# Optimization experiments

Hardware: AMD Instinct MI355X
Metric: run time of the kernel (lower is better)

Reference implementation:

```python
import math
import jax, jax.numpy as jnp
import numpy as np

H = 64  # lstm_hidden_size
T = 9   # seq_len


def _lstm_layer(pre, w_hh):
    """pre: [N, T, 4H] = x @ W_ih^T + b_ih + b_hh; w_hh: [4H, H].
    Returns full hidden sequence [N, T, H]. Gate order (PyTorch): i, f, g, o."""
    N = pre.shape[0]
    pre_t = jnp.transpose(pre, (1, 0, 2))  # [T, N, 4H]
    h0 = jnp.zeros((N, H), dtype=pre.dtype)
    c0 = jnp.zeros((N, H), dtype=pre.dtype)

    def step(carry, xt):
        h, c = carry
        g = xt + h @ w_hh.T  # [N, 4H]
        i = jax.nn.sigmoid(g[:, 0 * H:1 * H])
        f = jax.nn.sigmoid(g[:, 1 * H:2 * H])
        gg = jnp.tanh(g[:, 2 * H:3 * H])
        o = jax.nn.sigmoid(g[:, 3 * H:4 * H])
        c = f * c + i * gg
        h = o * jnp.tanh(c)
        return (h, c), h

    _, hs = jax.lax.scan(step, (h0, c0), pre_t)  # hs: [T, N, H]
    return jnp.transpose(hs, (1, 0, 2))  # [N, T, H]


def _forward(xy, w_ih0, w_hh0, b0, w_ih1, w_hh1, b1,
             fus_w, fus_b, res_w1, res_b1, res_w2, res_b2,
             head_w1, head_b1, head_w2, head_b2):
    x = xy[:, 0:1]
    y = xy[:, 1:2]
    pi = math.pi
    # seq: [N, 9, 1]
    seq = jnp.stack([x, y, x ** 2, y ** 2, x * y,
                     jnp.sin(pi * x), jnp.cos(pi * x),
                     jnp.sin(pi * y), jnp.cos(pi * y)], axis=1)
    # layer 0: input size 1
    pre0 = jnp.einsum('ntd,gd->ntg', seq, w_ih0) + b0  # [N, T, 4H]
    h_seq0 = _lstm_layer(pre0, w_hh0)                   # [N, T, H]
    # layer 1: input size H
    pre1 = jnp.einsum('nth,gh->ntg', h_seq0, w_ih1) + b1
    h_seq1 = _lstm_layer(pre1, w_hh1)
    feat = h_seq1[:, -1, :]                             # [N, H]

    fused = jnp.concatenate([feat, xy], axis=1)         # [N, H+2]
    z = jnp.tanh(fused @ fus_w.T + fus_b)               # [N, 64]
    for k in range(res_w1.shape[0]):
        t = jnp.tanh(z @ res_w1[k].T + res_b1[k])
        z = z + jnp.tanh(t @ res_w2[k].T + res_b2[k])
    h = jnp.tanh(z @ head_w1.T + head_b1)
    return h @ head_w2.T + head_b2                      # [N, 5]


def setup_inputs() -> dict:
    key = jax.random.key(0)
    ks = jax.random.split(key, 20)
    N = 262144
    D = 64  # fc_hidden_dim
    xy = jax.random.uniform(ks[0], (N, 2), dtype=jnp.float32)

    def w(k, shape, scale=0.1):
        return (jax.random.normal(k, shape, dtype=jnp.float32) * scale)

    inp = {
        'xy': xy,
        'w_ih0': w(ks[1], (4 * H, 1)),
        'w_hh0': w(ks[2], (4 * H, H)),
        'b0': jnp.zeros((4 * H,), jnp.float32),
        'w_ih1': w(ks[3], (4 * H, H)),
        'w_hh1': w(ks[4], (4 * H, H)),
        'b1': jnp.zeros((4 * H,), jnp.float32),
        'fus_w': w(ks[5], (D, H + 2)),
        'fus_b': jnp.zeros((D,), jnp.float32),
        'res_w1': w(ks[6], (3, D, D)),
        'res_b1': jnp.zeros((3, D), jnp.float32),
        'res_w2': w(ks[7], (3, D, D)),
        'res_b2': jnp.zeros((3, D), jnp.float32),
        'head_w1': w(ks[8], (D, D)),
        'head_b1': jnp.zeros((D,), jnp.float32),
        'head_w2': w(ks[9], (5, D)),
        'head_b2': jnp.zeros((5,), jnp.float32),
    }
    return inp


def reference(xy, w_ih0, w_hh0, b0, w_ih1, w_hh1, b1,
              fus_w, fus_b, res_w1, res_b1, res_w2, res_b2,
              head_w1, head_b1, head_w2, head_b2):
    return _forward(xy, w_ih0, w_hh0, b0, w_ih1, w_hh1, b1,
                    fus_w, fus_b, res_w1, res_b1, res_w2, res_b2,
                    head_w1, head_b1, head_w2, head_b2)
```

## Files before the change

### kernel.cpp

```cpp
#include <hip/hip_runtime.h>
#include <math.h>

#define PI_F 3.14159265358979323846f
#define WAVES 12
#define TPB (WAVES*64)
#define TPB2 512

typedef _Float16 half_t;
typedef __attribute__((ext_vector_type(8))) _Float16 f16x8;
typedef __attribute__((ext_vector_type(4))) float f32x4;

union F16x8U { f16x8 v; unsigned int u[4]; half_t h[8]; };

__device__ __forceinline__ float frcp(float x)  { return __builtin_amdgcn_rcpf(x); }
__device__ __forceinline__ float fsig(float x)  { return frcp(1.0f + __expf(-x)); }
__device__ __forceinline__ float ftanh(float x) { return 1.0f - 2.0f * frcp(1.0f + __expf(2.0f * x)); }

#define MFMA16(a,b,c) __builtin_amdgcn_mfma_f32_16x16x32_f16((a),(b),(c),0,0,0)

#define AUG_B   98304
#define B1_B    99328
#define EPI_H   50176
#define BIAS_B  172032
#define HOUT_H  88064
#define EF_FUS  0
#define EF_R1   6144
#define EF_R2   18432
#define EF_HW1  30720
#define EF_HW2  34816

__global__ void pack_weights(const float* __restrict__ w_ih0, const float* __restrict__ w_hh0, const float* __restrict__ b0,
                             const float* __restrict__ w_ih1, const float* __restrict__ w_hh1, const float* __restrict__ b1,
                             const float* __restrict__ fus_w, const float* __restrict__ fus_b,
                             const float* __restrict__ res_w1, const float* __restrict__ res_b1,
                             const float* __restrict__ res_w2, const float* __restrict__ res_b2,
                             const float* __restrict__ head_w1, const float* __restrict__ head_b1,
                             const float* __restrict__ head_w2, const float* __restrict__ head_b2,
                             half_t* __restrict__ hws)
{
    int id = blockIdx.x * blockDim.x + threadIdx.x;

    if (id < 6144) {
        int ln = id & 63, rest = id >> 6;
        int kb = rest & 1, cb = (rest >> 1) & 15, mat = rest >> 5;
        const float* W = (mat == 0) ? w_hh0 : ((mat == 1) ? w_ih1 : w_hh1);
        const float* src = W + (cb * 16 + (ln & 15)) * 64 + kb * 32 + (ln >> 4) * 8;
        F16x8U t;
        #pragma unroll
        for (int i = 0; i < 8; ++i) t.h[i] = (half_t)src[i];
        *(f16x8*)&hws[id * 8] = t.v;
        return;
    }
    id -= 6144;
    if (id < 256) {
        F16x8U t; t.u[0] = 0;
        t.h[0] = (half_t)w_ih0[id];
        t.h[1] = (half_t)b0[id];
        ((unsigned int*)((char*)hws + AUG_B))[id] = t.u[0];
        return;
    }
    id -= 256;
    if (id < 256) {
        ((float*)((char*)hws + B1_B))[id] = b1[id];
        return;
    }
    id -= 256;
    if (id < 768) {
        int ln = id & 63, rest = id >> 6;
        int kb = rest % 3, cb = rest / 3;
        int col = cb * 16 + (ln & 15), q = ln >> 4;
        F16x8U t; t.u[0] = t.u[1] = t.u[2] = t.u[3] = 0;
        if (kb < 2) {
            #pragma unroll
            for (int i = 0; i < 8; ++i) t.h[i] = (half_t)fus_w[col * 66 + kb * 32 + q * 8 + i];
        } else if (q == 0) {
            t.h[0] = (half_t)fus_w[col * 66 + 64];
            t.h[1] = (half_t)fus_w[col * 66 + 65];
            t.h[2] = (half_t)fus_b[col];
        }
        *(f16x8*)&hws[(EPI_H + EF_FUS + id * 8)] = t.v;
        return;
    }
    id -= 768;
    if (id < 1536) {
        int ln = id & 63, rest = id >> 6;
        int kb = rest & 1, cb = (rest >> 1) & 3, rb = rest >> 3;
        int col = cb * 16 + (ln & 15), q = ln >> 4;
        F16x8U t;
        #pragma unroll
        for (int i = 0; i < 8; ++i) t.h[i] = (half_t)res_w1[rb * 4096 + col * 64 + kb * 32 + q * 8 + i];
        *(f16x8*)&hws[(EPI_H + EF_R1 + id * 8)] = t.v;
        return;
    }
    id -= 1536;
    if (id < 1536) {
        int ln = id & 63, rest = id >> 6;
        int kb = rest & 1, cb = (rest >> 1) & 3, rb = rest >> 3;
        int col = cb * 16 + (ln & 15), q = ln >> 4;
        F16x8U t;
        #pragma unroll
        for (int i = 0; i < 8; ++i) t.h[i] = (half_t)res_w2[rb * 4096 + col * 64 + kb * 32 + q * 8 + i];
        *(f16x8*)&hws[(EPI_H + EF_R2 + id * 8)] = t.v;
        return;
    }
    id -= 1536;
    if (id < 512) {
        int ln = id & 63, rest = id >> 6;
        int kb = rest & 1, cb = rest >> 1;
        int col = cb * 16 + (ln & 15), q = ln >> 4;
        F16x8U t;
        #pragma unroll
        for (int i = 0; i < 8; ++i) t.h[i] = (half_t)head_w1[col * 64 + kb * 32 + q * 8 + i];
        *(f16x8*)&hws[(EPI_H + EF_HW1 + id * 8)] = t.v;
        return;
    }
    id -= 512;
    if (id < 128) {
        int ln = id & 63, kb = id >> 6;
        int col = ln & 15, q = ln >> 4;
        F16x8U t; t.u[0] = t.u[1] = t.u[2] = t.u[3] = 0;
        if (col < 5) {
            #pragma unroll
            for (int i = 0; i < 8; ++i) t.h[i] = (half_t)head_w2[col * 64 + kb * 32 + q * 8 + i];
        }
        *(f16x8*)&hws[(EPI_H + EF_HW2 + id * 8)] = t.v;
        return;
    }
    id -= 128;
    if (id < 517) {
        float v;
        if      (id < 64)  v = fus_b[id];
        else if (id < 256) v = res_b1[id - 64];
        else if (id < 448) v = res_b2[id - 256];
        else if (id < 512) v = head_b1[id - 448];
        else               v = head_b2[id - 512];
        ((float*)((char*)hws + BIAS_B))[id] = v;
        return;
    }
}

__global__ __launch_bounds__(TPB, 3)
void lstm_core(const float* __restrict__ xy, const half_t* __restrict__ hws, int N)
{
    __shared__ __align__(16) half_t wlds[3][16][2][64][8];
    __shared__ __align__(16) half_t hfrag[WAVES][2][2][64][8];
    __shared__ unsigned int aug_lds[256];
    __shared__ float b1_lds[256];

    const int lane = threadIdx.x & 63;
    const int wid  = threadIdx.x >> 6;
    const int cc   = lane & 15;
    const int qq   = lane >> 4;

    #pragma unroll
    for (int it = 0; it < 8; ++it) {
        int idx = threadIdx.x + it * TPB;
        *(f16x8*)&((half_t*)wlds)[idx * 8] = *(const f16x8*)&hws[idx * 8];
    }
    if (threadIdx.x < 256) {
        aug_lds[threadIdx.x] = ((const unsigned int*)((const char*)hws + AUG_B))[threadIdx.x];
        b1_lds[threadIdx.x]  = ((const float*)((const char*)hws + B1_B))[threadIdx.x];
    }
    __syncthreads();

    const int tile = blockIdx.x * WAVES + wid;
    const int S = tile * 16;
    if (S >= N) return;

    int si = S + cc; if (si >= N) si = N - 1;
    const float fx = xy[2 * si + 0];
    const float fy = xy[2 * si + 1];
    float feat[9];
    feat[0] = fx; feat[1] = fy; feat[2] = fx * fx; feat[3] = fy * fy; feat[4] = fx * fy;
    feat[5] = sinf(PI_F * fx); feat[6] = cosf(PI_F * fx);
    feat[7] = sinf(PI_F * fy); feat[8] = cosf(PI_F * fy);

    {
        F16x8U Z; Z.u[0] = Z.u[1] = Z.u[2] = Z.u[3] = 0;
        *(f16x8*)&hfrag[wid][0][0][lane][0] = Z.v;
        *(f16x8*)&hfrag[wid][0][1][lane][0] = Z.v;
        *(f16x8*)&hfrag[wid][1][0][lane][0] = Z.v;
        *(f16x8*)&hfrag[wid][1][1][lane][0] = Z.v;
    }
    float c0s[4][4], c1s[4][4];
    #pragma unroll
    for (int a = 0; a < 4; ++a)
        #pragma unroll
        for (int b = 0; b < 4; ++b) { c0s[a][b] = 0.0f; c1s[a][b] = 0.0f; }

    asm volatile("" ::: "memory");

    #pragma unroll 1
    for (int t = 0; t < 9; ++t) {
        float ftv;
        switch (t) {
            case 0: ftv = feat[0]; break;  case 1: ftv = feat[1]; break;
            case 2: ftv = feat[2]; break;  case 3: ftv = feat[3]; break;
            case 4: ftv = feat[4]; break;  case 5: ftv = feat[5]; break;
            case 6: ftv = feat[6]; break;  case 7: ftv = feat[7]; break;
            default: ftv = feat[8]; break;
        }
        F16x8U AG; AG.u[0] = AG.u[1] = AG.u[2] = AG.u[3] = 0;
        if (qq == 0) { AG.h[0] = (half_t)ftv; AG.h[1] = (half_t)1.0f; }

        f16x8 a00 = *(const f16x8*)&hfrag[wid][0][0][lane][0];
        f16x8 a01 = *(const f16x8*)&hfrag[wid][0][1][lane][0];
        #pragma unroll
        for (int jj = 0; jj < 4; ++jj) {
            f32x4 acc[4];
            #pragma unroll
            for (int g = 0; g < 4; ++g) {
                const int cb = jj + 4 * g;
                F16x8U BA; BA.u[0] = (qq == 0) ? aug_lds[cb * 16 + cc] : 0u;
                BA.u[1] = 0; BA.u[2] = 0; BA.u[3] = 0;
                f32x4 a = {0.f, 0.f, 0.f, 0.f};
                a = MFMA16(AG.v, BA.v, a);
                f16x8 bf0 = *(const f16x8*)&wlds[0][cb][0][lane][0];
                f16x8 bf1 = *(const f16x8*)&wlds[0][cb][1][lane][0];
                a = MFMA16(a00, bf0, a);
                a = MFMA16(a01, bf1, a);
                acc[g] = a;
            }
            const int kb = jj >> 1;
            half_t* hp = &hfrag[wid][0][kb][0][0];
            const int lb = (4 * qq + 16 * ((2 * jj + (cc >> 3)) & 3)) * 8 + (cc & 7);
            #pragma unroll
            for (int r = 0; r < 4; ++r) {
                float gi = fsig(acc[0][r]);
                float gf = fsig(acc[1][r]);
                float gg = ftanh(acc[2][r]);
                float go = fsig(acc[3][r]);
                float cv = gf * c0s[jj][r] + gi * gg;
                c0s[jj][r] = cv;
                hp[lb + 8 * r] = (half_t)(go * ftanh(cv));
            }
        }
        asm volatile("" ::: "memory");

        f16x8 a10 = *(const f16x8*)&hfrag[wid][0][0][lane][0];
        f16x8 a11 = *(const f16x8*)&hfrag[wid][0][1][lane][0];
        f16x8 a12 = *(const f16x8*)&hfrag[wid][1][0][lane][0];
        f16x8 a13 = *(const f16x8*)&hfrag[wid][1][1][lane][0];
        #pragma unroll
        for (int jj = 0; jj < 4; ++jj) {
            f32x4 acc[4];
            #pragma unroll
            for (int g = 0; g < 4; ++g) {
                const int cb = jj + 4 * g;
                const float bv = b1_lds[cb * 16 + cc];
                f32x4 a = {bv, bv, bv, bv};
                f16x8 bi0 = *(const f16x8*)&wlds[1][cb][0][lane][0];
                f16x8 bi1 = *(const f16x8*)&wlds[1][cb][1][lane][0];
                f16x8 bh0 = *(const f16x8*)&wlds[2][cb][0][lane][0];
                f16x8 bh1 = *(const f16x8*)&wlds[2][cb][1][lane][0];
                a = MFMA16(a10, bi0, a);
                a = MFMA16(a11, bi1, a);
                a = MFMA16(a12, bh0, a);
                a = MFMA16(a13, bh1, a);
                acc[g] = a;
            }
            const int kb = jj >> 1;
            half_t* hp = &hfrag[wid][1][kb][0][0];
            const int lb = (4 * qq + 16 * ((2 * jj + (cc >> 3)) & 3)) * 8 + (cc & 7);
            #pragma unroll
            for (int r = 0; r < 4; ++r) {
                float gi = fsig(acc[0][r]);
                float gf = fsig(acc[1][r]);
                float gg = ftanh(acc[2][r]);
                float go = fsig(acc[3][r]);
                float cv = gf * c1s[jj][r] + gi * gg;
                c1s[jj][r] = cv;
                hp[lb + 8 * r] = (half_t)(go * ftanh(cv));
            }
        }
        asm volatile("" ::: "memory");
    }

    half_t* hout = (half_t*)hws + HOUT_H + (size_t)tile * 1024;
    *(f16x8*)&hout[0   + lane * 8] = *(const f16x8*)&hfrag[wid][1][0][lane][0];
    *(f16x8*)&hout[512 + lane * 8] = *(const f16x8*)&hfrag[wid][1][1][lane][0];
}

__global__ __launch_bounds__(TPB2, 1)
void epi_mlp(const float* __restrict__ xy, const half_t* __restrict__ hws,
             float* __restrict__ out, int ntiles, int N)
{
    __shared__ __align__(16) half_t ef[35840];
    __shared__ float biasl[517];
    __shared__ __align__(16) half_t hbuf[8][2][2][64][8];

    for (int idx = threadIdx.x; idx < 4480; idx += TPB2)
        *(f16x8*)&ef[idx * 8] = *(const f16x8*)&hws[(EPI_H + idx * 8)];
    const float* bg = (const float*)((const char*)hws + BIAS_B);
    for (int i = threadIdx.x; i < 517; i += TPB2) biasl[i] = bg[i];
    __syncthreads();

    const half_t* hout = hws + HOUT_H;
    const int lane = threadIdx.x & 63;
    const int wid  = threadIdx.x >> 6;
    const int cc   = lane & 15;
    const int qq   = lane >> 4;
    const int gw = blockIdx.x * 8 + wid;
    const int nw = gridDim.x * 8;

#define WRITE_ACT(BUF, VALS) do {                                              \
        _Pragma("unroll")                                                      \
        for (int cb = 0; cb < 4; ++cb) {                                       \
            half_t* hp = &hbuf[wid][BUF][cb >> 1][0][0];                       \
            const int lb = (4*qq + 16*((2*cb + (cc>>3)) & 3))*8 + (cc & 7);    \
            _Pragma("unroll")                                                  \
            for (int r = 0; r < 4; ++r) hp[lb + 8*r] = (half_t)(VALS)[cb][r];  \
        }                                                                      \
        asm volatile("" ::: "memory");                                         \
    } while (0)

    #pragma unroll 1
    for (int tile = gw; tile < ntiles; tile += nw) {
        const size_t hob = (size_t)tile * 1024;
        f16x8 e0 = *(const f16x8*)&hout[hob + lane * 8];
        f16x8 e1 = *(const f16x8*)&hout[hob + 512 + lane * 8];

        int s = tile * 16 + cc; if (s >= N) s = N - 1;
        const float fx = xy[2 * s], fy = xy[2 * s + 1];
        F16x8U AF; AF.u[0] = AF.u[1] = AF.u[2] = AF.u[3] = 0;
        if (qq == 0) { AF.h[0] = (half_t)fx; AF.h[1] = (half_t)fy; AF.h[2] = (half_t)1.0f; }

        float zz[4][4];
        #pragma unroll
        for (int cb = 0; cb < 4; ++cb) {
            f32x4 a = {0.f, 0.f, 0.f, 0.f};
            a = MFMA16(e0,   *(const f16x8*)&ef[(EF_FUS + ((cb * 3 + 0) * 64 + lane) * 8)], a);
            a = MFMA16(e1,   *(const f16x8*)&ef[(EF_FUS + ((cb * 3 + 1) * 64 + lane) * 8)], a);
            a = MFMA16(AF.v, *(const f16x8*)&ef[(EF_FUS + ((cb * 3 + 2) * 64 + lane) * 8)], a);
            #pragma unroll
            for (int r = 0; r < 4; ++r) zz[cb][r] = ftanh(a[r]);
        }
        WRITE_ACT(0, zz);
        f16x8 za0 = *(const f16x8*)&hbuf[wid][0][0][lane][0];
        f16x8 za1 = *(const f16x8*)&hbuf[wid][0][1][lane][0];

        #pragma unroll 1
        for (int rb = 0; rb < 3; ++rb) {
            float tt[4][4];
            #pragma unroll
            for (int cb = 0; cb < 4; ++cb) {
                const float bv = biasl[64 + rb * 64 + cb * 16 + cc];
                f32x4 a = {bv, bv, bv, bv};
                a = MFMA16(za0, *(const f16x8*)&ef[(EF_R1 + (((rb * 4 + cb) * 2 + 0) * 64 + lane) * 8)], a);
                a = MFMA16(za1, *(const f16x8*)&ef[(EF_R1 + (((rb * 4 + cb) * 2 + 1) * 64 + lane) * 8)], a);
                #pragma unroll
                for (int r = 0; r < 4; ++r) tt[cb][r] = ftanh(a[r]);
            }
            WRITE_ACT(1, tt);
            f16x8 ta0 = *(const f16x8*)&hbuf[wid][1][0][lane][0];
            f16x8 ta1 = *(const f16x8*)&hbuf[wid][1][1][lane][0];
            #pragma unroll
            for (int cb = 0; cb < 4; ++cb) {
                const float bv = biasl[256 + rb * 64 + cb * 16 + cc];
                f32x4 a = {bv, bv, bv, bv};
                a = MFMA16(ta0, *(const f16x8*)&ef[(EF_R2 + (((rb * 4 + cb) * 2 + 0) * 64 + lane) * 8)], a);
                a = MFMA16(ta1, *(const f16x8*)&ef[(EF_R2 + (((rb * 4 + cb) * 2 + 1) * 64 + lane) * 8)], a);
                #pragma unroll
                for (int r = 0; r < 4; ++r) zz[cb][r] += ftanh(a[r]);
            }
            WRITE_ACT(0, zz);
            za0 = *(const f16x8*)&hbuf[wid][0][0][lane][0];
            za1 = *(const f16x8*)&hbuf[wid][0][1][lane][0];
        }

        float hh[4][4];
        #pragma unroll
        for (int cb = 0; cb < 4; ++cb) {
            const float bv = biasl[448 + cb * 16 + cc];
            f32x4 a = {bv, bv, bv, bv};
            a = MFMA16(za0, *(const f16x8*)&ef[(EF_HW1 + ((cb * 2 + 0) * 64 + lane) * 8)], a);
            a = MFMA16(za1, *(const f16x8*)&ef[(EF_HW1 + ((cb * 2 + 1) * 64 + lane) * 8)], a);
            #pragma unroll
            for (int r = 0; r < 4; ++r) hh[cb][r] = ftanh(a[r]);
        }
        WRITE_ACT(1, hh);
        f16x8 ha0 = *(const f16x8*)&hbuf[wid][1][0][lane][0];
        f16x8 ha1 = *(const f16x8*)&hbuf[wid][1][1][lane][0];

        {
            const float bv = (cc < 5) ? biasl[512 + cc] : 0.0f;
            f32x4 a = {bv, bv, bv, bv};
            a = MFMA16(ha0, *(const f16x8*)&ef[(EF_HW2 + ((0) * 64 + lane) * 8)], a);
            a = MFMA16(ha1, *(const f16x8*)&ef[(EF_HW2 + ((1) * 64 + lane) * 8)], a);
            if (cc < 5) {
                #pragma unroll
                for (int r = 0; r < 4; ++r) {
                    const int row = tile * 16 + 4 * qq + r;
                    if (row < N) out[row * 5 + cc] = a[r];
                }
            }
        }
    }
#undef WRITE_ACT
}

extern "C" void kernel_launch(void* const* d_in, const int* in_sizes, int n_in,
                              void* d_out, int out_size, void* d_ws, size_t ws_size,
                              hipStream_t stream) {
    const float* xy      = (const float*)d_in[0];
    const float* w_ih0   = (const float*)d_in[1];
    const float* w_hh0   = (const float*)d_in[2];
    const float* b0      = (const float*)d_in[3];
    const float* w_ih1   = (const float*)d_in[4];
    const float* w_hh1   = (const float*)d_in[5];
    const float* b1      = (const float*)d_in[6];
    const float* fus_w   = (const float*)d_in[7];
    const float* fus_b   = (const float*)d_in[8];
    const float* res_w1  = (const float*)d_in[9];
    const float* res_b1  = (const float*)d_in[10];
    const float* res_w2  = (const float*)d_in[11];
    const float* res_b2  = (const float*)d_in[12];
    const float* head_w1 = (const float*)d_in[13];
    const float* head_b1 = (const float*)d_in[14];
    const float* head_w2 = (const float*)d_in[15];
    const float* head_b2 = (const float*)d_in[16];

    const int N = in_sizes[0] / 2;
    const int ntiles = (N + 15) / 16;
    half_t* hws = (half_t*)d_ws;

    pack_weights<<<dim3(46), dim3(256), 0, stream>>>(
        w_ih0, w_hh0, b0, w_ih1, w_hh1, b1,
        fus_w, fus_b, res_w1, res_b1, res_w2, res_b2,
        head_w1, head_b1, head_w2, head_b2, hws);

    const int grid1 = (ntiles + WAVES - 1) / WAVES;
    lstm_core<<<dim3(grid1), dim3(TPB), 0, stream>>>(xy, hws, N);

    epi_mlp<<<dim3(256), dim3(TPB2), 0, stream>>>(xy, hws, (float*)d_out, ntiles, N);
}
```

Measured before the change: 549.6 us.

## Fuse LSTM gate math into fewer reciprocals and raise waves per block

Merges the sigmoid/tanh products in the LSTM cell update so that each i*g and o*tanh(c) pair needs one reciprocal instead of two, which cuts transcendental work. The aug and bias tables now live in per-lane registers instead of LDS, and the block grows from 12 to 15 waves with the launch-bounds occupancy hint raised from 3 to 4. In exchange the kernel carries more register pressure, and the product of denominators could overflow for large negative pre-activations.

```diff
diff --git a/kernel.cpp b/kernel.cpp
--- a/kernel.cpp
+++ b/kernel.cpp
@@ -2,7 +2,7 @@
 #include <math.h>
 
 #define PI_F 3.14159265358979323846f
-#define WAVES 12
+#define WAVES 15
 #define TPB (WAVES*64)
 #define TPB2 512
 
@@ -15,6 +15,19 @@
 __device__ __forceinline__ float frcp(float x)  { return __builtin_amdgcn_rcpf(x); }
 __device__ __forceinline__ float fsig(float x)  { return frcp(1.0f + __expf(-x)); }
 __device__ __forceinline__ float ftanh(float x) { return 1.0f - 2.0f * frcp(1.0f + __expf(2.0f * x)); }
+
+__device__ __forceinline__ float2 lstm_gate(float ai, float af, float ag, float ao, float cold) {
+    float ui = __expf(-ai);
+    float uf = __expf(-af);
+    float ug = __expf(-2.0f * ag);
+    float uo = __expf(-ao);
+    float ig = (1.0f - ug) * frcp((1.0f + ui) * (1.0f + ug));
+    float ff = frcp(1.0f + uf);
+    float cv = fmaf(ff, cold, ig);
+    float uc = __expf(-2.0f * cv);
+    float hh = (1.0f - uc) * frcp((1.0f + uo) * (1.0f + uc));
+    return make_float2(cv, hh);
+}
 
 #define MFMA16(a,b,c) __builtin_amdgcn_mfma_f32_16x16x32_f16((a),(b),(c),0,0,0)
 
@@ -139,29 +152,32 @@
     }
 }
 
-__global__ __launch_bounds__(TPB, 3)
+__global__ __launch_bounds__(TPB, 4)
 void lstm_core(const float* __restrict__ xy, const half_t* __restrict__ hws, int N)
 {
     __shared__ __align__(16) half_t wlds[3][16][2][64][8];
     __shared__ __align__(16) half_t hfrag[WAVES][2][2][64][8];
-    __shared__ unsigned int aug_lds[256];
-    __shared__ float b1_lds[256];
 
     const int lane = threadIdx.x & 63;
     const int wid  = threadIdx.x >> 6;
     const int cc   = lane & 15;
     const int qq   = lane >> 4;
 
-    #pragma unroll
-    for (int it = 0; it < 8; ++it) {
-        int idx = threadIdx.x + it * TPB;
+    for (int idx = threadIdx.x; idx < 6144; idx += TPB)
         *(f16x8*)&((half_t*)wlds)[idx * 8] = *(const f16x8*)&hws[idx * 8];
-    }
-    if (threadIdx.x < 256) {
-        aug_lds[threadIdx.x] = ((const unsigned int*)((const char*)hws + AUG_B))[threadIdx.x];
-        b1_lds[threadIdx.x]  = ((const float*)((const char*)hws + B1_B))[threadIdx.x];
-    }
     __syncthreads();
+
+    unsigned int augr[16];
+    float b1r[16];
+    {
+        const unsigned int* at = (const unsigned int*)((const char*)hws + AUG_B);
+        const float* bt = (const float*)((const char*)hws + B1_B);
+        #pragma unroll
+        for (int cb = 0; cb < 16; ++cb) {
+            augr[cb] = (qq == 0) ? at[cb * 16 + cc] : 0u;
+            b1r[cb]  = bt[cb * 16 + cc];
+        }
+    }
 
     const int tile = blockIdx.x * WAVES + wid;
     const int S = tile * 16;
@@ -211,8 +227,7 @@
             #pragma unroll
             for (int g = 0; g < 4; ++g) {
                 const int cb = jj + 4 * g;
-                F16x8U BA; BA.u[0] = (qq == 0) ? aug_lds[cb * 16 + cc] : 0u;
-                BA.u[1] = 0; BA.u[2] = 0; BA.u[3] = 0;
+                F16x8U BA; BA.u[0] = augr[cb]; BA.u[1] = 0; BA.u[2] = 0; BA.u[3] = 0;
                 f32x4 a = {0.f, 0.f, 0.f, 0.f};
                 a = MFMA16(AG.v, BA.v, a);
                 f16x8 bf0 = *(const f16x8*)&wlds[0][cb][0][lane][0];
@@ -226,13 +241,9 @@
             const int lb = (4 * qq + 16 * ((2 * jj + (cc >> 3)) & 3)) * 8 + (cc & 7);
             #pragma unroll
             for (int r = 0; r < 4; ++r) {
-                float gi = fsig(acc[0][r]);
-                float gf = fsig(acc[1][r]);
-                float gg = ftanh(acc[2][r]);
-                float go = fsig(acc[3][r]);
-                float cv = gf * c0s[jj][r] + gi * gg;
-                c0s[jj][r] = cv;
-                hp[lb + 8 * r] = (half_t)(go * ftanh(cv));
+                float2 ch = lstm_gate(acc[0][r], acc[1][r], acc[2][r], acc[3][r], c0s[jj][r]);
+                c0s[jj][r] = ch.x;
+                hp[lb + 8 * r] = (half_t)ch.y;
             }
         }
         asm volatile("" ::: "memory");
@@ -247,7 +258,7 @@
             #pragma unroll
             for (int g = 0; g < 4; ++g) {
                 const int cb = jj + 4 * g;
-                const float bv = b1_lds[cb * 16 + cc];
+                const float bv = b1r[cb];
                 f32x4 a = {bv, bv, bv, bv};
                 f16x8 bi0 = *(const f16x8*)&wlds[1][cb][0][lane][0];
                 f16x8 bi1 = *(const f16x8*)&wlds[1][cb][1][lane][0];
@@ -264,13 +275,9 @@
             const int lb = (4 * qq + 16 * ((2 * jj + (cc >> 3)) & 3)) * 8 + (cc & 7);
             #pragma unroll
             for (int r = 0; r < 4; ++r) {
-                float gi = fsig(acc[0][r]);
-                float gf = fsig(acc[1][r]);
-                float gg = ftanh(acc[2][r]);
-                float go = fsig(acc[3][r]);
-                float cv = gf * c1s[jj][r] + gi * gg;
-                c1s[jj][r] = cv;
-                hp[lb + 8 * r] = (half_t)(go * ftanh(cv));
+                float2 ch = lstm_gate(acc[0][r], acc[1][r], acc[2][r], acc[3][r], c1s[jj][r]);
+                c1s[jj][r] = ch.x;
+                hp[lb + 8 * r] = (half_t)ch.y;
             }
         }
         asm volatile("" ::: "memory");
```

Measured after the change: 755.1 us. 37.4% more time.
